# Optimization experiments

Hardware: AMD Instinct MI355X
Metric: run time of the kernel (lower is better)

Reference implementation:

```python
import jax, jax.numpy as jnp
import numpy as np

N, LH, PL = 512, 20, 10          # agents, history len, prediction len
H, E, NH, FF = 128, 64, 10, 2048  # rnn hidden, embedding, heads, ffn dim
D = H + 2                         # transformer d_model = 130
DH = D // NH                      # head dim = 13
DT = 0.1
NLAYERS = 3


def setup_inputs() -> dict:
    key = jax.random.key(0)
    ks = list(jax.random.split(key, 40))
    def rn(shape, s=0.02):
        return jax.random.normal(ks.pop(), shape, jnp.float32) * s
    Tracks = jax.random.normal(ks.pop(), (N, LH, 5), jnp.float32)
    Tracks = Tracks.at[:, :, 0].set(1.0)  # nonzero ids: all agents active every frame
    return dict(
        Tracks=Tracks,
        W_emb=rn((E, 4)), b_emb=jnp.zeros((E,), jnp.float32),
        W_ih=rn((4 * H, E)), W_hh=rn((4 * H, H)),
        b_ih=jnp.zeros((4 * H,), jnp.float32), b_hh=jnp.zeros((4 * H,), jnp.float32),
        enc_qkv_w=rn((NLAYERS, 3 * D, D)), enc_qkv_b=jnp.zeros((NLAYERS, 3 * D), jnp.float32),
        enc_out_w=rn((NLAYERS, D, D)), enc_out_b=jnp.zeros((NLAYERS, D), jnp.float32),
        enc_ff1_w=rn((NLAYERS, FF, D)), enc_ff1_b=jnp.zeros((NLAYERS, FF), jnp.float32),
        enc_ff2_w=rn((NLAYERS, D, FF)), enc_ff2_b=jnp.zeros((NLAYERS, D), jnp.float32),
        enc_ln1_s=jnp.ones((NLAYERS, D), jnp.float32), enc_ln1_b=jnp.zeros((NLAYERS, D), jnp.float32),
        enc_ln2_s=jnp.ones((NLAYERS, D), jnp.float32), enc_ln2_b=jnp.zeros((NLAYERS, D), jnp.float32),
        W_sp=rn((H, D)), b_sp=jnp.zeros((H,), jnp.float32),
        W_p1=rn((H, H)), b_p1=jnp.zeros((H,), jnp.float32),
        W_p2=rn((H, H)), b_p2=jnp.zeros((H,), jnp.float32),
        W_pl=rn((2, H)), b_pl=jnp.zeros((2,), jnp.float32),
    )


def _ln(x, s, b):
    m = jnp.mean(x, -1, keepdims=True)
    v = jnp.mean((x - m) ** 2, -1, keepdims=True)
    return (x - m) / jnp.sqrt(v + 1e-5) * s + b


def _mha(x, qkv_w, qkv_b, ow, ob):
    # x: [N, D] unbatched sequence of N agent tokens (torch unbatched semantics)
    qkv = x @ qkv_w.T + qkv_b
    q, k, v = jnp.split(qkv, 3, -1)
    def heads(t):
        return t.reshape(-1, NH, DH).transpose(1, 0, 2)  # [NH, N, DH]
    q, k, v = heads(q), heads(k), heads(v)
    scores = jnp.einsum('hnd,hmd->hnm', q, k) / jnp.sqrt(jnp.float32(DH))
    att = jax.nn.softmax(scores, -1)
    o = jnp.einsum('hnm,hmd->hnd', att, v).transpose(1, 0, 2).reshape(-1, D)
    return o @ ow.T + ob


def _forward(Tracks, W_emb, b_emb, W_ih, W_hh, b_ih, b_hh,
             enc_qkv_w, enc_qkv_b, enc_out_w, enc_out_b,
             enc_ff1_w, enc_ff1_b, enc_ff2_w, enc_ff2_b,
             enc_ln1_s, enc_ln1_b, enc_ln2_s, enc_ln2_b,
             W_sp, b_sp, W_p1, b_p1, W_p2, b_p2, W_pl, b_pl):
    def emb(x):
        return x @ W_emb.T + b_emb

    def lstm(x, h, c):  # torch LSTMCell, gate order i,f,g,o
        g = x @ W_ih.T + b_ih + h @ W_hh.T + b_hh
        i, f, gg, o = jnp.split(g, 4, -1)
        c2 = jax.nn.sigmoid(f) * c + jax.nn.sigmoid(i) * jnp.tanh(gg)
        return jax.nn.sigmoid(o) * jnp.tanh(c2), c2

    def sp(h, pos):  # sp_model: 3-layer post-norm transformer encoder + linear
        x = jnp.concatenate([h, pos], 1)  # [N, D]
        for j in range(NLAYERS):
            a = _mha(x, enc_qkv_w[j], enc_qkv_b[j], enc_out_w[j], enc_out_b[j])
            x = _ln(x + a, enc_ln1_s[j], enc_ln1_b[j])
            f = jax.nn.relu(x @ enc_ff1_w[j].T + enc_ff1_b[j]) @ enc_ff2_w[j].T + enc_ff2_b[j]
            x = _ln(x + f, enc_ln2_s[j], enc_ln2_b[j])
        return x @ W_sp.T + b_sp

    def rm_sp(inp, Sh, c):
        h2, c2 = lstm(emb(inp), Sh, c)
        return sp(h2, inp[:, :2]), c2

    n = Tracks.shape[0]
    inp0 = Tracks[:, 0, 1:]
    z = jnp.zeros((n, H), Tracks.dtype)
    h, c = lstm(emb(inp0), z, z)  # step-0 init (original processes step 0 twice)
    Sh = sp(h, inp0[:, :2])

    def step(carry, inp):
        Sh, c = carry
        Sh, c = rm_sp(inp, Sh, c)
        return (Sh, c), None

    (Sh, c), _ = jax.lax.scan(step, (Sh, c), jnp.moveaxis(Tracks[:, :, 1:], 1, 0))

    def pstep(carry, _):
        Sh, c, cf = carry
        x = jax.nn.relu(Sh @ W_p1.T + b_p1) + Sh
        x = jax.nn.relu(x @ W_p2.T + b_p2) + x
        a = x @ W_pl.T + b_pl                       # acceleration [N,2]
        v = a * DT + cf[:, 2:]                      # velocity update first (in-place order)
        pnew = a * (DT * DT / 2) + v * DT + cf[:, :2]
        out = jnp.concatenate([pnew, v], 1)
        Sh, c = rm_sp(out, Sh, c)
        return (Sh, c, out), out

    _, pre = jax.lax.scan(pstep, (Sh, c, Tracks[:, -1, 1:]), None, length=PL)
    return jnp.moveaxis(pre, 0, 1)  # [N, pre_len, 4]


def reference(Tracks, W_emb, b_emb, W_ih, W_hh, b_ih, b_hh,
              enc_qkv_w, enc_qkv_b, enc_out_w, enc_out_b,
              enc_ff1_w, enc_ff1_b, enc_ff2_w, enc_ff2_b,
              enc_ln1_s, enc_ln1_b, enc_ln2_s, enc_ln2_b,
              W_sp, b_sp, W_p1, b_p1, W_p2, b_p2, W_pl, b_pl):
    return _forward(Tracks, W_emb, b_emb, W_ih, W_hh, b_ih, b_hh,
                    enc_qkv_w, enc_qkv_b, enc_out_w, enc_out_b,
                    enc_ff1_w, enc_ff1_b, enc_ff2_w, enc_ff2_b,
                    enc_ln1_s, enc_ln1_b, enc_ln2_s, enc_ln2_b,
                    W_sp, b_sp, W_p1, b_p1, W_p2, b_p2, W_pl, b_pl)
```

## Files before the change

kernel.cpp:

```cpp
#include <hip/hip_runtime.h>


#define Nn 512
#define Dd 130
#define DP 132
#define Hh 128
#define Ee 64
#define FFf 2048
#define KG 192
#define TS 68

typedef float v4 __attribute__((ext_vector_type(4)));
typedef float v2 __attribute__((ext_vector_type(2)));

struct Args {
  const float *Tracks, *W_emb, *b_emb, *W_ih, *W_hh, *b_ih, *b_hh;
  const float *qkv_w, *qkv_b, *out_w, *out_b, *ff1_w, *ff1_b, *ff2_w, *ff2_b;
  const float *ln1_s, *ln1_b, *ln2_s, *ln2_b;
  const float *W_sp, *b_sp, *W_p1, *b_p1, *W_p2, *b_p2, *W_pl, *b_pl;
  float *X, *T, *Q, *Kb, *V, *O, *Sh, *C, *X1, *X2, *Y, *PART, *outp;
};

__device__ __forceinline__ float sigm(float x){ return 1.f/(1.f+__expf(-x)); }

__global__ __launch_bounds__(512) void k_proj(Args a){
  int rg = blockIdx.x & 7, cs = blockIdx.x >> 3;
  int r0 = rg*64, c0 = cs*64;
  __shared__ alignas(16) float xs[Dd*TS];
  __shared__ alignas(16) float ws[Dd*TS];
  int tid = threadIdx.x, cg = tid & 15, ig = tid >> 4;
  for (int idx=tid; idx<64*Dd; idx+=512){ int i=idx/Dd, j=idx-i*Dd; xs[j*TS+i] = a.X[(r0+i)*DP+j]; }
  for (int idx=tid; idx<64*Dd; idx+=512){ int c=idx/Dd, j=idx-c*Dd; ws[j*TS+c] = a.W_sp[(c0+c)*Dd+j]; }
  __syncthreads();
  float acc[2][4] = {};
  const float* xp = xs + 2*ig;
  const float* wp = ws + 4*cg;
  #pragma unroll 4
  for (int j=0;j<Dd;j++){
    v2 xv = *(const v2*)(xp + j*TS);
    v4 wv = *(const v4*)(wp + j*TS);
    #pragma unroll
    for (int aa=0;aa<2;aa++)
      #pragma unroll
      for (int bb=0;bb<4;bb++) acc[aa][bb] += xv[aa]*wv[bb];
  }
  #pragma unroll
  for (int aa=0;aa<2;aa++){
    int r = r0 + 2*ig + aa, c = c0 + 4*cg;
    v4 o; 
    #pragma unroll
    for (int bb=0;bb<4;bb++) o[bb] = acc[aa][bb] + a.b_sp[c+bb];
    *(v4*)&a.Sh[r*Hh+c] = o;
  }
}

__global__ __launch_bounds__(512) void k_mlp(Args a, const float* inp, const float* W, const float* b, float* outp){
  int rg = blockIdx.x & 7, cs = blockIdx.x >> 3;
  int r0 = rg*64, c0 = cs*64;
  __shared__ alignas(16) float xs[Hh*TS];
  __shared__ alignas(16) float ws[Hh*TS];
  int tid = threadIdx.x, cg = tid & 15, ig = tid >> 4;
  for (int idx=tid; idx<64*Hh; idx+=512){ int i=idx>>7, j=idx&127; xs[j*TS+i] = inp[(r0+i)*Hh+j]; }
  for (int idx=tid; idx<64*Hh; idx+=512){ int c=idx>>7, j=idx&127; ws[j*TS+c] = W[(c0+c)*Hh+j]; }
  __syncthreads();
  float acc[2][4] = {};
  const float* xp = xs + 2*ig;
  const float* wp = ws + 4*cg;
  #pragma unroll 4
  for (int j=0;j<Hh;j++){
    v2 xv = *(const v2*)(xp + j*TS);
    v4 wv = *(const v4*)(wp + j*TS);
    #pragma unroll
    for (int aa=0;aa<2;aa++)
      #pragma unroll
      for (int bb=0;bb<4;bb++) acc[aa][bb] += xv[aa]*wv[bb];
  }
  #pragma unroll
  for (int aa=0;aa<2;aa++){
    int r = r0 + 2*ig + aa, c = c0 + 4*cg;
    v4 ri = *(const v4*)&inp[r*Hh+c];
    v4 o;
    #pragma unroll
    for (int bb=0;bb<4;bb++) o[bb] = fmaxf(acc[aa][bb]+b[c+bb],0.f) + ri[bb];
    *(v4*)&outp[r*Hh+c] = o;
  }
}

__global__ __launch_bounds__(256) void k_pout(Args a, int p){
  int r0 = blockIdx.x*8;
  __shared__ float red[16*17];
  int tid = threadIdx.x;
  int o = tid & 15, kq = tid >> 4;
  int ii = o>>1, jj = o&1, r = r0+ii;
  float s = 0.f;
  for (int v=kq*8; v<kq*8+8; v++) s += a.X2[r*Hh+v]*a.W_pl[jj*Hh+v];
  red[o*17+kq] = s;
  __syncthreads();
  if (tid < 16){
    int oo=tid, i2=oo>>1, j=oo&1, rr=r0+i2;
    float av = a.b_pl[j];
    for (int k=0;k<16;k++) av += red[oo*17+k];
    float cf0, cf2;
    if (p==0){ cf0 = a.Tracks[(rr*20+19)*5+1+j]; cf2 = a.Tracks[(rr*20+19)*5+3+j]; }
    else     { cf0 = a.outp[rr*40+(p-1)*4+j];    cf2 = a.outp[rr*40+(p-1)*4+2+j]; }
    float vv = av*0.1f + cf2;
    float pn = av*0.005f + vv*0.1f + cf0;
    a.outp[rr*40+p*4+j]   = pn;
    a.outp[rr*40+p*4+2+j] = vv;
  }
}

__global__ __launch_bounds__(512) void k_gates(Args a, int xin_mode, int tstep, int p, int sh_zero){
  int rg = blockIdx.x & 7, us = blockIdx.x >> 3;
  int r0 = rg*64, u0 = us*16;
  __shared__ alignas(16) float xs[KG*TS];
  __shared__ alignas(16) float ws[KG*TS];
  __shared__ float xin[64*4];
  int tid = threadIdx.x, cg = tid & 15, ig = tid >> 4;
  for (int idx=tid; idx<64*4; idx+=512){ int i=idx>>2, j=idx&3; int r=r0+i;
    xin[i*4+j] = (xin_mode==0) ? a.Tracks[(r*20+tstep)*5+1+j] : a.outp[r*40+p*4+j]; }
  for (int idx=tid; idx<64*Hh; idx+=512){ int i=idx>>7, v=idx&127;
    xs[(Ee+v)*TS+i] = sh_zero ? 0.f : a.Sh[(r0+i)*Hh+v]; }
  for (int idx=tid; idx<64*KG; idx+=512){ int row=idx/KG, j=idx-row*KG;
    int u=row>>2, g=row&3; int wrow = g*Hh + u0 + u;
    ws[j*TS+row] = (j<Ee) ? a.W_ih[wrow*Ee+j] : a.W_hh[wrow*Hh+(j-Ee)]; }
  __syncthreads();
  for (int idx=tid; idx<64*Ee; idx+=512){ int e=idx>>6, i=idx&63;
    float s = a.b_emb[e];
    #pragma unroll
    for (int j=0;j<4;j++) s += xin[i*4+j]*a.W_emb[e*4+j];
    xs[e*TS+i] = s; }
  __syncthreads();
  float acc[2][4] = {};
  const float* xp = xs + 2*ig;
  const float* wp = ws + 4*cg;
  #pragma unroll 4
  for (int j=0;j<KG;j++){
    v2 xv = *(const v2*)(xp + j*TS);
    v4 wv = *(const v4*)(wp + j*TS);
    #pragma unroll
    for (int aa=0;aa<2;aa++)
      #pragma unroll
      for (int bb=0;bb<4;bb++) acc[aa][bb] += xv[aa]*wv[bb];
  }
  int u = u0 + cg;
  #pragma unroll
  for (int rr=0;rr<2;rr++){
    int r = r0 + 2*ig + rr;
    float gi = acc[rr][0] + a.b_ih[u]      + a.b_hh[u];
    float gf = acc[rr][1] + a.b_ih[Hh+u]   + a.b_hh[Hh+u];
    float gg = acc[rr][2] + a.b_ih[2*Hh+u] + a.b_hh[2*Hh+u];
    float go = acc[rr][3] + a.b_ih[3*Hh+u] + a.b_hh[3*Hh+u];
    float cp = sh_zero ? 0.f : a.C[r*Hh+u];
    float c2 = sigm(gf)*cp + sigm(gi)*tanhf(gg);
    a.C[r*Hh+u] = c2;
    a.X[r*DP+u] = sigm(go)*tanhf(c2);
  }
  if (us==0 && tid<128){ int i=tid>>1, jj=tid&1;
    a.X[(r0+i)*DP + Hh + jj] = xin[i*4+jj]; }
}

__global__ __launch_bounds__(512) void k_qkv(Args a, int layer){
  int rg = blockIdx.x & 7, cs = blockIdx.x >> 3;
  int r0 = rg*64, c0 = cs*64;
  __shared__ alignas(16) float xs[Dd*TS];
  __shared__ alignas(16) float ws[Dd*TS];
  const float* qw = a.qkv_w + layer*390*Dd;
  const float* qb = a.qkv_b + layer*390;
  int tid = threadIdx.x, cg = tid & 15, ig = tid >> 4;
  for (int idx=tid; idx<64*Dd; idx+=512){ int i=idx/Dd, j=idx-i*Dd; xs[j*TS+i] = a.X[(r0+i)*DP+j]; }
  for (int idx=tid; idx<64*Dd; idx+=512){ int c=idx/Dd, j=idx-c*Dd; int gc=c0+c;
    ws[j*TS+c] = (gc<390) ? qw[gc*Dd+j] : 0.f; }
  __syncthreads();
  float acc[2][4] = {};
  const float* xp = xs + 2*ig;
  const float* wp = ws + 4*cg;
  #pragma unroll 4
  for (int j=0;j<Dd;j++){
    v2 xv = *(const v2*)(xp + j*TS);
    v4 wv = *(const v4*)(wp + j*TS);
    #pragma unroll
    for (int aa=0;aa<2;aa++)
      #pragma unroll
      for (int bb=0;bb<4;bb++) acc[aa][bb] += xv[aa]*wv[bb];
  }
  #pragma unroll
  for (int aa=0;aa<2;aa++){
    int r = r0 + 2*ig + aa;
    #pragma unroll
    for (int bb=0;bb<4;bb++){
      int c = c0 + 4*cg + bb;
      if (c < 390){
        float v = acc[aa][bb] + qb[c];
        if (c < Dd)        a.Q [r*DP + c]        = v;
        else if (c < 2*Dd) a.Kb[r*DP + (c-Dd)]   = v;
        else               a.V [r*DP + (c-2*Dd)] = v;
      }
    }
  }
}

__global__ __launch_bounds__(256) void k_attn(Args a){
  int rg = blockIdx.x & 31, head = blockIdx.x >> 5;
  int r0 = rg*16, hc = head*13;
  __shared__ alignas(16) float kv[512*14];
  __shared__ alignas(16) float sc[16*516];
  __shared__ float red[16*17];
  __shared__ float rowm[16], rowsi[16];
  int tid = threadIdx.x;
  const float scale = rsqrtf(13.f);
  for (int idx=tid; idx<512*13; idx+=256){ int m=idx/13, d=idx-13*m; kv[m*14+d]=a.Kb[m*DP+hc+d]; }
  __syncthreads();
  { int ii=tid>>4, mg=tid&15;
    float q[13];
    #pragma unroll
    for (int d=0;d<13;d++) q[d]=a.Q[(r0+ii)*DP+hc+d]*scale;
    for (int k=0;k<32;k++){ int m=mg+16*k;
      float s=0.f;
      #pragma unroll
      for (int d=0;d<13;d++) s += q[d]*kv[m*14+d];
      sc[ii*516+m]=s; } }
  __syncthreads();
  for (int idx=tid; idx<512*13; idx+=256){ int m=idx/13, d=idx-13*m; kv[d*524+m]=a.V[m*DP+hc+d]; }
  { int row=tid>>4, l=tid&15; float mx=-1e30f;
    for (int k=0;k<32;k++) mx=fmaxf(mx, sc[row*516+l+16*k]);
    red[row*17+l]=mx; }
  __syncthreads();
  if (tid<16){ float mx=-1e30f; for(int k=0;k<16;k++) mx=fmaxf(mx,red[tid*17+k]); rowm[tid]=mx; }
  __syncthreads();
  { int row=tid>>4, l=tid&15; float s=0.f; float mx=rowm[row];
    for (int k=0;k<32;k++){ int m=l+16*k; float e=__expf(sc[row*516+m]-mx); sc[row*516+m]=e; s+=e; }
    red[row*17+l]=s; }
  __syncthreads();
  if (tid<16){ float s=0.f; for(int k=0;k<16;k++) s+=red[tid*17+k]; rowsi[tid]=1.f/s; }
  __syncthreads();
  if (tid<208){ int ii=tid/13, d=tid-13*ii;
    float accv=0.f;
    const float* sp = sc + ii*516;
    const float* vp = kv + d*524;
    #pragma unroll 4
    for (int mb=0;mb<128;mb++){
      v4 sv = *(const v4*)(sp + 4*mb);
      v4 vv = *(const v4*)(vp + 4*mb);
      accv += sv[0]*vv[0]+sv[1]*vv[1]+sv[2]*vv[2]+sv[3]*vv[3];
    }
    a.O[(r0+ii)*DP+hc+d]=accv*rowsi[ii]; }
}

__global__ __launch_bounds__(512) void k_oproj(Args a, int layer){
  int rg = blockIdx.x & 7, cs = blockIdx.x >> 3;
  int r0 = rg*64, c0 = cs*64;
  __shared__ alignas(16) float xs[Dd*TS];
  __shared__ alignas(16) float ws[Dd*TS];
  const float* ow = a.out_w + layer*Dd*Dd;
  const float* ob = a.out_b + layer*Dd;
  int tid = threadIdx.x, cg = tid & 15, ig = tid >> 4;
  for (int idx=tid; idx<64*Dd; idx+=512){ int i=idx/Dd, j=idx-i*Dd; xs[j*TS+i]=a.O[(r0+i)*DP+j]; }
  for (int idx=tid; idx<64*Dd; idx+=512){ int c=idx/Dd, j=idx-c*Dd; int gc=c0+c;
    ws[j*TS+c] = (gc<Dd) ? ow[gc*Dd+j] : 0.f; }
  __syncthreads();
  float acc[2][4] = {};
  const float* xp = xs + 2*ig;
  const float* wp = ws + 4*cg;
  #pragma unroll 4
  for (int j=0;j<Dd;j++){
    v2 xv = *(const v2*)(xp + j*TS);
    v4 wv = *(const v4*)(wp + j*TS);
    #pragma unroll
    for (int aa=0;aa<2;aa++)
      #pragma unroll
      for (int bb=0;bb<4;bb++) acc[aa][bb] += xv[aa]*wv[bb];
  }
  #pragma unroll
  for (int aa=0;aa<2;aa++){
    int r = r0 + 2*ig + aa;
    #pragma unroll
    for (int bb=0;bb<4;bb++){
      int c = c0 + 4*cg + bb;
      if (c < Dd) a.T[r*DP+c] = acc[aa][bb] + ob[c] + a.X[r*DP+c];
    }
  }
}

__global__ __launch_bounds__(256) void k_ln(Args a, const float* s, const float* b, int mode_ff, int layer){
  int r0 = blockIdx.x*8;
  __shared__ float row[8*132];
  __shared__ float red1[8*33], red2[8*33];
  __shared__ float mu[8], inv[8];
  int tid = threadIdx.x, i = tid>>5, l = tid&31;
  if (mode_ff==0){
    for (int idx=tid; idx<8*Dd; idx+=256){ int ii=idx/Dd, c=idx-ii*Dd; row[ii*132+c]=a.T[(r0+ii)*DP+c]; }
  } else {
    const float* f2b = a.ff2_b + layer*Dd;
    for (int idx=tid; idx<8*Dd; idx+=256){ int ii=idx/Dd, c=idx-ii*Dd;
      float sum = a.X[(r0+ii)*DP+c] + f2b[c];
      for (int ksl=0;ksl<16;ksl++) sum += a.PART[(ksl*Nn + r0+ii)*DP + c];
      row[ii*132+c]=sum; }
  }
  __syncthreads();
  { float s1=0.f, s2=0.f;
    for (int k=0;k<5;k++){ int c=l+32*k; if(c<Dd){ float v=row[i*132+c]; s1+=v; s2+=v*v; } }
    red1[i*33+l]=s1; red2[i*33+l]=s2; }
  __syncthreads();
  if (tid<8){ float s1=0.f,s2=0.f; for(int k=0;k<32;k++){ s1+=red1[tid*33+k]; s2+=red2[tid*33+k]; }
    float m=s1/130.f; mu[tid]=m; inv[tid]=rsqrtf(s2/130.f - m*m + 1e-5f); }
  __syncthreads();
  for (int idx=tid; idx<8*Dd; idx+=256){ int ii=idx/Dd, c=idx-ii*Dd;
    a.X[(r0+ii)*DP+c] = (row[ii*132+c]-mu[ii])*inv[ii]*s[c] + b[c]; }
}

__global__ __launch_bounds__(512) void k_ff1(Args a, int layer){
  int rg = blockIdx.x & 7, cs = blockIdx.x >> 3;
  int r0 = rg*64, c0 = cs*64;
  __shared__ alignas(16) float xs[Dd*TS];
  __shared__ alignas(16) float ws[Dd*TS];
  const float* w1 = a.ff1_w + layer*FFf*Dd;
  const float* b1 = a.ff1_b + layer*FFf;
  int tid = threadIdx.x, cg = tid & 15, ig = tid >> 4;
  for (int idx=tid; idx<64*Dd; idx+=512){ int i=idx/Dd, j=idx-i*Dd; xs[j*TS+i]=a.X[(r0+i)*DP+j]; }
  for (int idx=tid; idx<64*Dd; idx+=512){ int c=idx/Dd, j=idx-c*Dd; ws[j*TS+c]=w1[(c0+c)*Dd+j]; }
  __syncthreads();
  float acc[2][4] = {};
  const float* xp = xs + 2*ig;
  const float* wp = ws + 4*cg;
  #pragma unroll 4
  for (int j=0;j<Dd;j++){
    v2 xv = *(const v2*)(xp + j*TS);
    v4 wv = *(const v4*)(wp + j*TS);
    #pragma unroll
    for (int aa=0;aa<2;aa++)
      #pragma unroll
      for (int bb=0;bb<4;bb++) acc[aa][bb] += xv[aa]*wv[bb];
  }
  #pragma unroll
  for (int aa=0;aa<2;aa++){
    int r = r0 + 2*ig + aa, c = c0 + 4*cg;
    v4 o;
    #pragma unroll
    for (int bb=0;bb<4;bb++) o[bb] = fmaxf(acc[aa][bb]+b1[c+bb],0.f);
    *(v4*)&a.Y[r*FFf+c] = o;
  }
}

__global__ __launch_bounds__(512) void k_ff2(Args a, int layer){
  int b = blockIdx.x;
  int rg = b & 7; int t = b >> 3; int ks = t/3; int cs = t - ks*3;
  int r0 = rg*64, c0 = cs*64, k0 = ks*128;
  __shared__ alignas(16) float xs[128*TS];
  __shared__ alignas(16) float ws[128*TS];
  const float* w2 = a.ff2_w + layer*Dd*FFf;
  int tid = threadIdx.x, cg = tid & 15, ig = tid >> 4;
  for (int idx=tid; idx<64*128; idx+=512){ int i=idx>>7, j=idx&127; xs[j*TS+i]=a.Y[(r0+i)*FFf+k0+j]; }
  for (int idx=tid; idx<64*128; idx+=512){ int c=idx>>7, j=idx&127; int gc=c0+c;
    ws[j*TS+c] = (gc<Dd) ? w2[gc*FFf+k0+j] : 0.f; }
  __syncthreads();
  float acc[2][4] = {};
  const float* xp = xs + 2*ig;
  const float* wp = ws + 4*cg;
  #pragma unroll 4
  for (int j=0;j<128;j++){
    v2 xv = *(const v2*)(xp + j*TS);
    v4 wv = *(const v4*)(wp + j*TS);
    #pragma unroll
    for (int aa=0;aa<2;aa++)
      #pragma unroll
      for (int bb=0;bb<4;bb++) acc[aa][bb] += xv[aa]*wv[bb];
  }
  #pragma unroll
  for (int aa=0;aa<2;aa++){
    int r = r0 + 2*ig + aa;
    #pragma unroll
    for (int bb=0;bb<4;bb++){
      int c = c0 + 4*cg + bb;
      if (c < Dd) a.PART[(ks*Nn + r)*DP + c] = acc[aa][bb];
    }
  }
}

extern "C" void kernel_launch(void* const* d_in, const int* in_sizes, int n_in,
                              void* d_out, int out_size, void* d_ws, size_t ws_size,
                              hipStream_t stream) {
  (void)in_sizes; (void)n_in; (void)out_size; (void)ws_size;
  Args A;
  const float* const* in = (const float* const*)d_in;
  A.Tracks=in[0]; A.W_emb=in[1]; A.b_emb=in[2]; A.W_ih=in[3]; A.W_hh=in[4]; A.b_ih=in[5]; A.b_hh=in[6];
  A.qkv_w=in[7]; A.qkv_b=in[8]; A.out_w=in[9]; A.out_b=in[10];
  A.ff1_w=in[11]; A.ff1_b=in[12]; A.ff2_w=in[13]; A.ff2_b=in[14];
  A.ln1_s=in[15]; A.ln1_b=in[16]; A.ln2_s=in[17]; A.ln2_b=in[18];
  A.W_sp=in[19]; A.b_sp=in[20]; A.W_p1=in[21]; A.b_p1=in[22]; A.W_p2=in[23]; A.b_p2=in[24];
  A.W_pl=in[25]; A.b_pl=in[26];
  float* ws = (float*)d_ws;
  A.X   = ws;
  A.T   = ws + 67584;
  A.Q   = ws + 135168;
  A.Kb  = ws + 202752;
  A.V   = ws + 270336;
  A.O   = ws + 337920;
  A.Sh  = ws + 405504;
  A.C   = ws + 471040;
  A.X1  = ws + 536576;
  A.X2  = ws + 602112;
  A.Y   = ws + 667648;
  A.PART= ws + 1716224;
  A.outp = (float*)d_out;

  dim3 B5(512), B2(256);
  auto enc = [&](){
    for (int l=0;l<3;l++){
      k_qkv  <<<dim3(56),  B5, 0, stream>>>(A, l);
      k_attn <<<dim3(320), B2, 0, stream>>>(A);
      k_oproj<<<dim3(24),  B5, 0, stream>>>(A, l);
      k_ln   <<<dim3(64),  B2, 0, stream>>>(A, A.ln1_s+l*Dd, A.ln1_b+l*Dd, 0, l);
      k_ff1  <<<dim3(256), B5, 0, stream>>>(A, l);
      k_ff2  <<<dim3(384), B5, 0, stream>>>(A, l);
      k_ln   <<<dim3(64),  B2, 0, stream>>>(A, A.ln2_s+l*Dd, A.ln2_b+l*Dd, 1, l);
    }
  };

  k_gates<<<dim3(64), B5, 0, stream>>>(A, 0, 0, 0, 1);
  enc();
  for (int t=0;t<20;t++){
    k_proj <<<dim3(16), B5, 0, stream>>>(A);
    k_gates<<<dim3(64), B5, 0, stream>>>(A, 0, t, 0, 0);
    enc();
  }
  for (int p=0;p<10;p++){
    k_proj<<<dim3(16), B5, 0, stream>>>(A);
    k_mlp <<<dim3(16), B5, 0, stream>>>(A, A.Sh, A.W_p1, A.b_p1, A.X1);
    k_mlp <<<dim3(16), B5, 0, stream>>>(A, A.X1, A.W_p2, A.b_p2, A.X2);
    k_pout<<<dim3(64), B2, 0, stream>>>(A, p);
    if (p < 9){
      k_gates<<<dim3(64), B5, 0, stream>>>(A, 1, 0, p, 0);
      enc();
    }
  }
}
```

Measured before the change: 9.059 ms.

## Fuse all stage kernels into one persistent kernel with grid-wide barriers

Replaces the long sequence of small kernel launches (hundreds per forward) with a single persistent 256-block kernel. Each former kernel becomes a device phase that loops over virtual blocks, with an atomic-counter grid barrier between phases. Attention now uses 512 threads with split reductions, and ff2 uses a 2-chunk K split to halve partial sums. This removes launch overhead and inter-kernel gaps. In exchange every phase pays a spin-wait barrier, and small phases leave most blocks idle at lower occupancy (one 512-thread block per CU).

```diff
diff --git a/kernel.cpp b/kernel.cpp
--- a/kernel.cpp
+++ b/kernel.cpp
@@ -7,8 +7,9 @@
 #define Hh 128
 #define Ee 64
 #define FFf 2048
-#define KG 192
 #define TS 68
+#define NB 256
+#define NT 512
 
 typedef float v4 __attribute__((ext_vector_type(4)));
 typedef float v2 __attribute__((ext_vector_type(2)));
@@ -19,18 +20,19 @@
   const float *ln1_s, *ln1_b, *ln2_s, *ln2_b;
   const float *W_sp, *b_sp, *W_p1, *b_p1, *W_p2, *b_p2, *W_pl, *b_pl;
   float *X, *T, *Q, *Kb, *V, *O, *Sh, *C, *X1, *X2, *Y, *PART, *outp;
+  unsigned *bar;
 };
 
 __device__ __forceinline__ float sigm(float x){ return 1.f/(1.f+__expf(-x)); }
 
-__global__ __launch_bounds__(512) void k_proj(Args a){
-  int rg = blockIdx.x & 7, cs = blockIdx.x >> 3;
+__device__ __forceinline__ void ph_proj(const Args& a, float* sm, int vb){
+  int rg = vb & 7, cs = vb >> 3;
   int r0 = rg*64, c0 = cs*64;
-  __shared__ alignas(16) float xs[Dd*TS];
-  __shared__ alignas(16) float ws[Dd*TS];
-  int tid = threadIdx.x, cg = tid & 15, ig = tid >> 4;
-  for (int idx=tid; idx<64*Dd; idx+=512){ int i=idx/Dd, j=idx-i*Dd; xs[j*TS+i] = a.X[(r0+i)*DP+j]; }
-  for (int idx=tid; idx<64*Dd; idx+=512){ int c=idx/Dd, j=idx-c*Dd; ws[j*TS+c] = a.W_sp[(c0+c)*Dd+j]; }
+  float* xs = sm; float* ws = sm + 13056;
+  int tid = threadIdx.x, cg = tid & 15, ig = tid >> 4;
+  __syncthreads();
+  for (int idx=tid; idx<64*Dd; idx+=NT){ int i=idx/Dd, j=idx-i*Dd; xs[j*TS+i] = a.X[(r0+i)*DP+j]; }
+  for (int idx=tid; idx<64*Dd; idx+=NT){ int c=idx/Dd, j=idx-c*Dd; ws[j*TS+c] = a.W_sp[(c0+c)*Dd+j]; }
   __syncthreads();
   float acc[2][4] = {};
   const float* xp = xs + 2*ig;
@@ -47,21 +49,22 @@
   #pragma unroll
   for (int aa=0;aa<2;aa++){
     int r = r0 + 2*ig + aa, c = c0 + 4*cg;
-    v4 o; 
+    v4 o;
     #pragma unroll
     for (int bb=0;bb<4;bb++) o[bb] = acc[aa][bb] + a.b_sp[c+bb];
     *(v4*)&a.Sh[r*Hh+c] = o;
   }
 }
 
-__global__ __launch_bounds__(512) void k_mlp(Args a, const float* inp, const float* W, const float* b, float* outp){
-  int rg = blockIdx.x & 7, cs = blockIdx.x >> 3;
+__device__ __forceinline__ void ph_mlp(const Args& a, float* sm, int vb,
+                                       const float* inp, const float* W, const float* b, float* outp){
+  int rg = vb & 7, cs = vb >> 3;
   int r0 = rg*64, c0 = cs*64;
-  __shared__ alignas(16) float xs[Hh*TS];
-  __shared__ alignas(16) float ws[Hh*TS];
-  int tid = threadIdx.x, cg = tid & 15, ig = tid >> 4;
-  for (int idx=tid; idx<64*Hh; idx+=512){ int i=idx>>7, j=idx&127; xs[j*TS+i] = inp[(r0+i)*Hh+j]; }
-  for (int idx=tid; idx<64*Hh; idx+=512){ int c=idx>>7, j=idx&127; ws[j*TS+c] = W[(c0+c)*Hh+j]; }
+  float* xs = sm; float* ws = sm + 13056;
+  int tid = threadIdx.x, cg = tid & 15, ig = tid >> 4;
+  __syncthreads();
+  for (int idx=tid; idx<64*Hh; idx+=NT){ int i=idx>>7, j=idx&127; xs[j*TS+i] = inp[(r0+i)*Hh+j]; }
+  for (int idx=tid; idx<64*Hh; idx+=NT){ int c=idx>>7, j=idx&127; ws[j*TS+c] = W[(c0+c)*Hh+j]; }
   __syncthreads();
   float acc[2][4] = {};
   const float* xp = xs + 2*ig;
@@ -86,15 +89,18 @@
   }
 }
 
-__global__ __launch_bounds__(256) void k_pout(Args a, int p){
-  int r0 = blockIdx.x*8;
-  __shared__ float red[16*17];
+__device__ __forceinline__ void ph_pout(const Args& a, float* sm, int vb, int p){
+  float* red = sm;
+  int r0 = vb*8;
   int tid = threadIdx.x;
-  int o = tid & 15, kq = tid >> 4;
-  int ii = o>>1, jj = o&1, r = r0+ii;
-  float s = 0.f;
-  for (int v=kq*8; v<kq*8+8; v++) s += a.X2[r*Hh+v]*a.W_pl[jj*Hh+v];
-  red[o*17+kq] = s;
+  __syncthreads();
+  if (tid < 256){
+    int o = tid & 15, kq = tid >> 4;
+    int ii = o>>1, jj = o&1, r = r0+ii;
+    float s = 0.f;
+    for (int v=kq*8; v<kq*8+8; v++) s += a.X2[r*Hh+v]*a.W_pl[jj*Hh+v];
+    red[o*17+kq] = s;
+  }
   __syncthreads();
   if (tid < 16){
     int oo=tid, i2=oo>>1, j=oo&1, rr=r0+i2;
@@ -110,38 +116,47 @@
   }
 }
 
-__global__ __launch_bounds__(512) void k_gates(Args a, int xin_mode, int tstep, int p, int sh_zero){
-  int rg = blockIdx.x & 7, us = blockIdx.x >> 3;
+__device__ __forceinline__ void ph_gates(const Args& a, float* sm, int vb,
+                                         int xin_mode, int tstep, int p, int sh_zero){
+  int rg = vb & 7, us = vb >> 3;
   int r0 = rg*64, u0 = us*16;
-  __shared__ alignas(16) float xs[KG*TS];
-  __shared__ alignas(16) float ws[KG*TS];
-  __shared__ float xin[64*4];
-  int tid = threadIdx.x, cg = tid & 15, ig = tid >> 4;
-  for (int idx=tid; idx<64*4; idx+=512){ int i=idx>>2, j=idx&3; int r=r0+i;
+  float* xs = sm;
+  float* ws = sm + 6528;
+  float* xin = sm + 13056;
+  int tid = threadIdx.x, cg = tid & 15, ig = tid >> 4;
+  __syncthreads();
+  for (int idx=tid; idx<64*4; idx+=NT){ int i=idx>>2, j=idx&3; int r=r0+i;
     xin[i*4+j] = (xin_mode==0) ? a.Tracks[(r*20+tstep)*5+1+j] : a.outp[r*40+p*4+j]; }
-  for (int idx=tid; idx<64*Hh; idx+=512){ int i=idx>>7, v=idx&127;
-    xs[(Ee+v)*TS+i] = sh_zero ? 0.f : a.Sh[(r0+i)*Hh+v]; }
-  for (int idx=tid; idx<64*KG; idx+=512){ int row=idx/KG, j=idx-row*KG;
-    int u=row>>2, g=row&3; int wrow = g*Hh + u0 + u;
-    ws[j*TS+row] = (j<Ee) ? a.W_ih[wrow*Ee+j] : a.W_hh[wrow*Hh+(j-Ee)]; }
-  __syncthreads();
-  for (int idx=tid; idx<64*Ee; idx+=512){ int e=idx>>6, i=idx&63;
-    float s = a.b_emb[e];
-    #pragma unroll
-    for (int j=0;j<4;j++) s += xin[i*4+j]*a.W_emb[e*4+j];
-    xs[e*TS+i] = s; }
-  __syncthreads();
-  float acc[2][4] = {};
-  const float* xp = xs + 2*ig;
-  const float* wp = ws + 4*cg;
-  #pragma unroll 4
-  for (int j=0;j<KG;j++){
-    v2 xv = *(const v2*)(xp + j*TS);
-    v4 wv = *(const v4*)(wp + j*TS);
-    #pragma unroll
-    for (int aa=0;aa<2;aa++)
-      #pragma unroll
-      for (int bb=0;bb<4;bb++) acc[aa][bb] += xv[aa]*wv[bb];
+  float acc[2][4] = {};
+  for (int ch=0; ch<2; ch++){
+    __syncthreads();
+    for (int idx=tid; idx<96*64; idx+=NT){ int kk=idx>>6, i=idx&63; int k=ch*96+kk;
+      float v;
+      if (k < Ee){
+        v = a.b_emb[k];
+        #pragma unroll
+        for (int j=0;j<4;j++) v += xin[i*4+j]*a.W_emb[k*4+j];
+      } else {
+        v = sh_zero ? 0.f : a.Sh[(r0+i)*Hh + (k-Ee)];
+      }
+      xs[kk*TS+i] = v;
+    }
+    for (int idx=tid; idx<96*64; idx+=NT){ int kk=idx>>6, row=idx&63; int k=ch*96+kk;
+      int u=row>>2, g=row&3; int wrow = g*Hh + u0 + u;
+      ws[kk*TS+row] = (k<Ee) ? a.W_ih[wrow*Ee+k] : a.W_hh[wrow*Hh+(k-Ee)];
+    }
+    __syncthreads();
+    const float* xp = xs + 2*ig;
+    const float* wp = ws + 4*cg;
+    #pragma unroll 4
+    for (int jj=0;jj<96;jj++){
+      v2 xv = *(const v2*)(xp + jj*TS);
+      v4 wv = *(const v4*)(wp + jj*TS);
+      #pragma unroll
+      for (int aa=0;aa<2;aa++)
+        #pragma unroll
+        for (int bb=0;bb<4;bb++) acc[aa][bb] += xv[aa]*wv[bb];
+    }
   }
   int u = u0 + cg;
   #pragma unroll
@@ -160,16 +175,16 @@
     a.X[(r0+i)*DP + Hh + jj] = xin[i*4+jj]; }
 }
 
-__global__ __launch_bounds__(512) void k_qkv(Args a, int layer){
-  int rg = blockIdx.x & 7, cs = blockIdx.x >> 3;
+__device__ __forceinline__ void ph_qkv(const Args& a, float* sm, int vb, int layer){
+  int rg = vb & 7, cs = vb >> 3;
   int r0 = rg*64, c0 = cs*64;
-  __shared__ alignas(16) float xs[Dd*TS];
-  __shared__ alignas(16) float ws[Dd*TS];
+  float* xs = sm; float* ws = sm + 13056;
   const float* qw = a.qkv_w + layer*390*Dd;
   const float* qb = a.qkv_b + layer*390;
   int tid = threadIdx.x, cg = tid & 15, ig = tid >> 4;
-  for (int idx=tid; idx<64*Dd; idx+=512){ int i=idx/Dd, j=idx-i*Dd; xs[j*TS+i] = a.X[(r0+i)*DP+j]; }
-  for (int idx=tid; idx<64*Dd; idx+=512){ int c=idx/Dd, j=idx-c*Dd; int gc=c0+c;
+  __syncthreads();
+  for (int idx=tid; idx<64*Dd; idx+=NT){ int i=idx/Dd, j=idx-i*Dd; xs[j*TS+i] = a.X[(r0+i)*DP+j]; }
+  for (int idx=tid; idx<64*Dd; idx+=NT){ int c=idx/Dd, j=idx-c*Dd; int gc=c0+c;
     ws[j*TS+c] = (gc<390) ? qw[gc*Dd+j] : 0.f; }
   __syncthreads();
   float acc[2][4] = {};
@@ -200,63 +215,69 @@
   }
 }
 
-__global__ __launch_bounds__(256) void k_attn(Args a){
-  int rg = blockIdx.x & 31, head = blockIdx.x >> 5;
+__device__ __forceinline__ void ph_attn(const Args& a, float* sm, int vb){
+  float* kv    = sm;
+  float* sc    = sm + 7168;
+  float* red   = sm + 15424;
+  float* rowm  = sm + 15952;
+  float* rowsi = sm + 15968;
+  float* red2  = sm + 15984;
+  int rg = vb & 31, head = vb >> 5;
   int r0 = rg*16, hc = head*13;
-  __shared__ alignas(16) float kv[512*14];
-  __shared__ alignas(16) float sc[16*516];
-  __shared__ float red[16*17];
-  __shared__ float rowm[16], rowsi[16];
   int tid = threadIdx.x;
   const float scale = rsqrtf(13.f);
-  for (int idx=tid; idx<512*13; idx+=256){ int m=idx/13, d=idx-13*m; kv[m*14+d]=a.Kb[m*DP+hc+d]; }
-  __syncthreads();
-  { int ii=tid>>4, mg=tid&15;
+  __syncthreads();
+  for (int idx=tid; idx<512*13; idx+=NT){ int m=idx/13, d=idx-13*m; kv[m*14+d]=a.Kb[m*DP+hc+d]; }
+  __syncthreads();
+  { int ii=tid>>5, mg=tid&31;
     float q[13];
     #pragma unroll
     for (int d=0;d<13;d++) q[d]=a.Q[(r0+ii)*DP+hc+d]*scale;
-    for (int k=0;k<32;k++){ int m=mg+16*k;
+    for (int k=0;k<16;k++){ int m=mg+32*k;
       float s=0.f;
       #pragma unroll
       for (int d=0;d<13;d++) s += q[d]*kv[m*14+d];
       sc[ii*516+m]=s; } }
   __syncthreads();
-  for (int idx=tid; idx<512*13; idx+=256){ int m=idx/13, d=idx-13*m; kv[d*524+m]=a.V[m*DP+hc+d]; }
-  { int row=tid>>4, l=tid&15; float mx=-1e30f;
-    for (int k=0;k<32;k++) mx=fmaxf(mx, sc[row*516+l+16*k]);
-    red[row*17+l]=mx; }
-  __syncthreads();
-  if (tid<16){ float mx=-1e30f; for(int k=0;k<16;k++) mx=fmaxf(mx,red[tid*17+k]); rowm[tid]=mx; }
-  __syncthreads();
-  { int row=tid>>4, l=tid&15; float s=0.f; float mx=rowm[row];
-    for (int k=0;k<32;k++){ int m=l+16*k; float e=__expf(sc[row*516+m]-mx); sc[row*516+m]=e; s+=e; }
-    red[row*17+l]=s; }
-  __syncthreads();
-  if (tid<16){ float s=0.f; for(int k=0;k<16;k++) s+=red[tid*17+k]; rowsi[tid]=1.f/s; }
-  __syncthreads();
-  if (tid<208){ int ii=tid/13, d=tid-13*ii;
+  for (int idx=tid; idx<512*13; idx+=NT){ int m=idx/13, d=idx-13*m; kv[d*524+m]=a.V[m*DP+hc+d]; }
+  { int row=tid>>5, l=tid&31; float mx=-1e30f;
+    for (int k=0;k<16;k++) mx=fmaxf(mx, sc[row*516+l+32*k]);
+    red[row*33+l]=mx; }
+  __syncthreads();
+  if (tid<16){ float mx=-1e30f; for(int k=0;k<32;k++) mx=fmaxf(mx,red[tid*33+k]); rowm[tid]=mx; }
+  __syncthreads();
+  { int row=tid>>5, l=tid&31; float s=0.f; float mx=rowm[row];
+    for (int k=0;k<16;k++){ int m=l+32*k; float e=__expf(sc[row*516+m]-mx); sc[row*516+m]=e; s+=e; }
+    red[row*33+l]=s; }
+  __syncthreads();
+  if (tid<16){ float s=0.f; for(int k=0;k<32;k++) s+=red[tid*33+k]; rowsi[tid]=1.f/s; }
+  __syncthreads();
+  if (tid<416){ int pid=tid>>1, h=tid&1; int ii=pid/13, d=pid-13*ii;
+    const float* sp = sc + ii*516 + h*256;
+    const float* vp = kv + d*524 + h*256;
     float accv=0.f;
-    const float* sp = sc + ii*516;
-    const float* vp = kv + d*524;
     #pragma unroll 4
-    for (int mb=0;mb<128;mb++){
+    for (int mb=0;mb<64;mb++){
       v4 sv = *(const v4*)(sp + 4*mb);
       v4 vv = *(const v4*)(vp + 4*mb);
       accv += sv[0]*vv[0]+sv[1]*vv[1]+sv[2]*vv[2]+sv[3]*vv[3];
     }
-    a.O[(r0+ii)*DP+hc+d]=accv*rowsi[ii]; }
-}
-
-__global__ __launch_bounds__(512) void k_oproj(Args a, int layer){
-  int rg = blockIdx.x & 7, cs = blockIdx.x >> 3;
+    red2[pid*2+h]=accv; }
+  __syncthreads();
+  if (tid<208){ int ii=tid/13, d=tid-13*ii;
+    a.O[(r0+ii)*DP+hc+d]=(red2[tid*2]+red2[tid*2+1])*rowsi[ii]; }
+}
+
+__device__ __forceinline__ void ph_oproj(const Args& a, float* sm, int vb, int layer){
+  int rg = vb & 7, cs = vb >> 3;
   int r0 = rg*64, c0 = cs*64;
-  __shared__ alignas(16) float xs[Dd*TS];
-  __shared__ alignas(16) float ws[Dd*TS];
+  float* xs = sm; float* ws = sm + 13056;
   const float* ow = a.out_w + layer*Dd*Dd;
   const float* ob = a.out_b + layer*Dd;
   int tid = threadIdx.x, cg = tid & 15, ig = tid >> 4;
-  for (int idx=tid; idx<64*Dd; idx+=512){ int i=idx/Dd, j=idx-i*Dd; xs[j*TS+i]=a.O[(r0+i)*DP+j]; }
-  for (int idx=tid; idx<64*Dd; idx+=512){ int c=idx/Dd, j=idx-c*Dd; int gc=c0+c;
+  __syncthreads();
+  for (int idx=tid; idx<64*Dd; idx+=NT){ int i=idx/Dd, j=idx-i*Dd; xs[j*TS+i]=a.O[(r0+i)*DP+j]; }
+  for (int idx=tid; idx<64*Dd; idx+=NT){ int c=idx/Dd, j=idx-c*Dd; int gc=c0+c;
     ws[j*TS+c] = (gc<Dd) ? ow[gc*Dd+j] : 0.f; }
   __syncthreads();
   float acc[2][4] = {};
@@ -282,43 +303,50 @@
   }
 }
 
-__global__ __launch_bounds__(256) void k_ln(Args a, const float* s, const float* b, int mode_ff, int layer){
-  int r0 = blockIdx.x*8;
-  __shared__ float row[8*132];
-  __shared__ float red1[8*33], red2[8*33];
-  __shared__ float mu[8], inv[8];
-  int tid = threadIdx.x, i = tid>>5, l = tid&31;
+__device__ __forceinline__ void ph_ln(const Args& a, float* sm, int vb,
+                                      const float* s, const float* b, int mode_ff, int layer){
+  float* row  = sm;
+  float* red1 = sm + 1056;
+  float* red2 = sm + 1320;
+  float* mu   = sm + 1584;
+  float* inv  = sm + 1592;
+  int r0 = vb*8;
+  int tid = threadIdx.x;
+  __syncthreads();
   if (mode_ff==0){
-    for (int idx=tid; idx<8*Dd; idx+=256){ int ii=idx/Dd, c=idx-ii*Dd; row[ii*132+c]=a.T[(r0+ii)*DP+c]; }
+    for (int idx=tid; idx<8*Dd; idx+=NT){ int ii=idx/Dd, c=idx-ii*Dd; row[ii*132+c]=a.T[(r0+ii)*DP+c]; }
   } else {
     const float* f2b = a.ff2_b + layer*Dd;
-    for (int idx=tid; idx<8*Dd; idx+=256){ int ii=idx/Dd, c=idx-ii*Dd;
+    for (int idx=tid; idx<8*Dd; idx+=NT){ int ii=idx/Dd, c=idx-ii*Dd;
       float sum = a.X[(r0+ii)*DP+c] + f2b[c];
-      for (int ksl=0;ksl<16;ksl++) sum += a.PART[(ksl*Nn + r0+ii)*DP + c];
+      for (int ksl=0;ksl<8;ksl++) sum += a.PART[(ksl*Nn + r0+ii)*DP + c];
       row[ii*132+c]=sum; }
   }
   __syncthreads();
-  { float s1=0.f, s2=0.f;
+  if (tid<256){
+    int i = tid>>5, l = tid&31;
+    float s1=0.f, s2=0.f;
     for (int k=0;k<5;k++){ int c=l+32*k; if(c<Dd){ float v=row[i*132+c]; s1+=v; s2+=v*v; } }
-    red1[i*33+l]=s1; red2[i*33+l]=s2; }
+    red1[i*33+l]=s1; red2[i*33+l]=s2;
+  }
   __syncthreads();
   if (tid<8){ float s1=0.f,s2=0.f; for(int k=0;k<32;k++){ s1+=red1[tid*33+k]; s2+=red2[tid*33+k]; }
     float m=s1/130.f; mu[tid]=m; inv[tid]=rsqrtf(s2/130.f - m*m + 1e-5f); }
   __syncthreads();
-  for (int idx=tid; idx<8*Dd; idx+=256){ int ii=idx/Dd, c=idx-ii*Dd;
+  for (int idx=tid; idx<8*Dd; idx+=NT){ int ii=idx/Dd, c=idx-ii*Dd;
     a.X[(r0+ii)*DP+c] = (row[ii*132+c]-mu[ii])*inv[ii]*s[c] + b[c]; }
 }
 
-__global__ __launch_bounds__(512) void k_ff1(Args a, int layer){
-  int rg = blockIdx.x & 7, cs = blockIdx.x >> 3;
+__device__ __forceinline__ void ph_ff1(const Args& a, float* sm, int vb, int layer){
+  int rg = vb & 7, cs = vb >> 3;
   int r0 = rg*64, c0 = cs*64;
-  __shared__ alignas(16) float xs[Dd*TS];
-  __shared__ alignas(16) float ws[Dd*TS];
+  float* xs = sm; float* ws = sm + 13056;
   const float* w1 = a.ff1_w + layer*FFf*Dd;
   const float* b1 = a.ff1_b + layer*FFf;
   int tid = threadIdx.x, cg = tid & 15, ig = tid >> 4;
-  for (int idx=tid; idx<64*Dd; idx+=512){ int i=idx/Dd, j=idx-i*Dd; xs[j*TS+i]=a.X[(r0+i)*DP+j]; }
-  for (int idx=tid; idx<64*Dd; idx+=512){ int c=idx/Dd, j=idx-c*Dd; ws[j*TS+c]=w1[(c0+c)*Dd+j]; }
+  __syncthreads();
+  for (int idx=tid; idx<64*Dd; idx+=NT){ int i=idx/Dd, j=idx-i*Dd; xs[j*TS+i]=a.X[(r0+i)*DP+j]; }
+  for (int idx=tid; idx<64*Dd; idx+=NT){ int c=idx/Dd, j=idx-c*Dd; ws[j*TS+c]=w1[(c0+c)*Dd+j]; }
   __syncthreads();
   float acc[2][4] = {};
   const float* xp = xs + 2*ig;
@@ -342,29 +370,31 @@
   }
 }
 
-__global__ __launch_bounds__(512) void k_ff2(Args a, int layer){
-  int b = blockIdx.x;
-  int rg = b & 7; int t = b >> 3; int ks = t/3; int cs = t - ks*3;
-  int r0 = rg*64, c0 = cs*64, k0 = ks*128;
-  __shared__ alignas(16) float xs[128*TS];
-  __shared__ alignas(16) float ws[128*TS];
+__device__ __forceinline__ void ph_ff2(const Args& a, float* sm, int vb, int layer){
+  int rg = vb & 7; int t = vb >> 3; int ks = t/3; int cs = t - ks*3;
+  int r0 = rg*64, c0 = cs*64, k0 = ks*256;
+  float* xs = sm; float* ws = sm + 13056;
   const float* w2 = a.ff2_w + layer*Dd*FFf;
   int tid = threadIdx.x, cg = tid & 15, ig = tid >> 4;
-  for (int idx=tid; idx<64*128; idx+=512){ int i=idx>>7, j=idx&127; xs[j*TS+i]=a.Y[(r0+i)*FFf+k0+j]; }
-  for (int idx=tid; idx<64*128; idx+=512){ int c=idx>>7, j=idx&127; int gc=c0+c;
-    ws[j*TS+c] = (gc<Dd) ? w2[gc*FFf+k0+j] : 0.f; }
-  __syncthreads();
-  float acc[2][4] = {};
-  const float* xp = xs + 2*ig;
-  const float* wp = ws + 4*cg;
-  #pragma unroll 4
-  for (int j=0;j<128;j++){
-    v2 xv = *(const v2*)(xp + j*TS);
-    v4 wv = *(const v4*)(wp + j*TS);
-    #pragma unroll
-    for (int aa=0;aa<2;aa++)
-      #pragma unroll
-      for (int bb=0;bb<4;bb++) acc[aa][bb] += xv[aa]*wv[bb];
+  float acc[2][4] = {};
+  for (int ch=0; ch<2; ch++){
+    __syncthreads();
+    int kb = k0 + ch*128;
+    for (int idx=tid; idx<64*128; idx+=NT){ int i=idx>>7, j=idx&127; xs[j*TS+i]=a.Y[(r0+i)*FFf+kb+j]; }
+    for (int idx=tid; idx<64*128; idx+=NT){ int c=idx>>7, j=idx&127; int gc=c0+c;
+      ws[j*TS+c] = (gc<Dd) ? w2[gc*FFf+kb+j] : 0.f; }
+    __syncthreads();
+    const float* xp = xs + 2*ig;
+    const float* wp = ws + 4*cg;
+    #pragma unroll 4
+    for (int j=0;j<128;j++){
+      v2 xv = *(const v2*)(xp + j*TS);
+      v4 wv = *(const v4*)(wp + j*TS);
+      #pragma unroll
+      for (int aa=0;aa<2;aa++)
+        #pragma unroll
+        for (int bb=0;bb<4;bb++) acc[aa][bb] += xv[aa]*wv[bb];
+    }
   }
   #pragma unroll
   for (int aa=0;aa<2;aa++){
@@ -373,6 +403,58 @@
     for (int bb=0;bb<4;bb++){
       int c = c0 + 4*cg + bb;
       if (c < Dd) a.PART[(ks*Nn + r)*DP + c] = acc[aa][bb];
+    }
+  }
+}
+
+#define FORVB(G) for (int vb = (int)blockIdx.x; vb < (G); vb += NB)
+
+__global__ __launch_bounds__(NT, 1) void mega(Args a){
+  __shared__ float sm[21896];
+  unsigned tgt = 0;
+  unsigned* bar = a.bar;
+
+  auto GSYNC = [&](){
+    __syncthreads();
+    if (threadIdx.x == 0){
+      tgt += NB;
+      __threadfence();
+      __hip_atomic_fetch_add(bar, 1u, __ATOMIC_RELAXED, __HIP_MEMORY_SCOPE_AGENT);
+      while (__hip_atomic_load(bar, __ATOMIC_RELAXED, __HIP_MEMORY_SCOPE_AGENT) < tgt){
+        __builtin_amdgcn_s_sleep(1);
+      }
+      __threadfence();
+    }
+    __syncthreads();
+  };
+
+  auto enc = [&](){
+    for (int l=0;l<3;l++){
+      FORVB(56)  ph_qkv  (a, sm, vb, l);                                   GSYNC();
+      FORVB(320) ph_attn (a, sm, vb);                                      GSYNC();
+      FORVB(24)  ph_oproj(a, sm, vb, l);                                   GSYNC();
+      FORVB(64)  ph_ln   (a, sm, vb, a.ln1_s+l*Dd, a.ln1_b+l*Dd, 0, l);    GSYNC();
+      FORVB(256) ph_ff1  (a, sm, vb, l);                                   GSYNC();
+      FORVB(192) ph_ff2  (a, sm, vb, l);                                   GSYNC();
+      FORVB(64)  ph_ln   (a, sm, vb, a.ln2_s+l*Dd, a.ln2_b+l*Dd, 1, l);    GSYNC();
+    }
+  };
+
+  FORVB(64) ph_gates(a, sm, vb, 0, 0, 0, 1);  GSYNC();
+  enc();
+  for (int t=0;t<20;t++){
+    FORVB(16) ph_proj (a, sm, vb);            GSYNC();
+    FORVB(64) ph_gates(a, sm, vb, 0, t, 0, 0); GSYNC();
+    enc();
+  }
+  for (int p=0;p<10;p++){
+    FORVB(16) ph_proj(a, sm, vb);                                  GSYNC();
+    FORVB(16) ph_mlp (a, sm, vb, a.Sh, a.W_p1, a.b_p1, a.X1);      GSYNC();
+    FORVB(16) ph_mlp (a, sm, vb, a.X1, a.W_p2, a.b_p2, a.X2);      GSYNC();
+    FORVB(64) ph_pout(a, sm, vb, p);                               GSYNC();
+    if (p < 9){
+      FORVB(64) ph_gates(a, sm, vb, 1, 0, p, 0);                   GSYNC();
+      enc();
     }
   }
 }
@@ -402,36 +484,9 @@
   A.X2  = ws + 602112;
   A.Y   = ws + 667648;
   A.PART= ws + 1716224;
+  A.bar = (unsigned*)(ws + 2256896);
   A.outp = (float*)d_out;
 
-  dim3 B5(512), B2(256);
-  auto enc = [&](){
-    for (int l=0;l<3;l++){
-      k_qkv  <<<dim3(56),  B5, 0, stream>>>(A, l);
-      k_attn <<<dim3(320), B2, 0, stream>>>(A);
-      k_oproj<<<dim3(24),  B5, 0, stream>>>(A, l);
-      k_ln   <<<dim3(64),  B2, 0, stream>>>(A, A.ln1_s+l*Dd, A.ln1_b+l*Dd, 0, l);
-      k_ff1  <<<dim3(256), B5, 0, stream>>>(A, l);
-      k_ff2  <<<dim3(384), B5, 0, stream>>>(A, l);
-      k_ln   <<<dim3(64),  B2, 0, stream>>>(A, A.ln2_s+l*Dd, A.ln2_b+l*Dd, 1, l);
-    }
-  };
-
-  k_gates<<<dim3(64), B5, 0, stream>>>(A, 0, 0, 0, 1);
-  enc();
-  for (int t=0;t<20;t++){
-    k_proj <<<dim3(16), B5, 0, stream>>>(A);
-    k_gates<<<dim3(64), B5, 0, stream>>>(A, 0, t, 0, 0);
-    enc();
-  }
-  for (int p=0;p<10;p++){
-    k_proj<<<dim3(16), B5, 0, stream>>>(A);
-    k_mlp <<<dim3(16), B5, 0, stream>>>(A, A.Sh, A.W_p1, A.b_p1, A.X1);
-    k_mlp <<<dim3(16), B5, 0, stream>>>(A, A.X1, A.W_p2, A.b_p2, A.X2);
-    k_pout<<<dim3(64), B2, 0, stream>>>(A, p);
-    if (p < 9){
-      k_gates<<<dim3(64), B5, 0, stream>>>(A, 1, 0, p, 0);
-      enc();
-    }
-  }
-}
+  hipMemsetAsync((void*)A.bar, 0, 64, stream);
+  mega<<<dim3(NB), dim3(NT), 0, stream>>>(A);
+}
```

After: 21.54 ms. 2.38x slower.

## Fuse layernorms into FF1 and projection kernels, halve FF2 split-K

Applied to the files above, without the earlier changes.

The post-attention layernorm is folded into the FF1 kernel. Each block recomputes the norm for its 64 rows, and the first column slice writes the normalized X back. The last encoder layer's FF2-reduction layernorm moves into the spatial projection kernel, so two launches per encoder pass are removed. FF2 now covers 256 K-columns per block in two chunks, which halves the split-K partial count and the partial sums reduced afterward. The cost is redundant LN work across column blocks, extra shared memory that may lower occupancy, and fewer FF2 blocks.

```diff
diff --git a/kernel.cpp b/kernel.cpp
--- a/kernel.cpp
+++ b/kernel.cpp
@@ -23,14 +23,36 @@
 
 __device__ __forceinline__ float sigm(float x){ return 1.f/(1.f+__expf(-x)); }
 
+#define LN_REDUCE(SCR) \
+  { int row_=tid>>3, l8=tid&7; float s1=0.f, s2=0.f; \
+    for (int k=0;k<17;k++){ int c=l8+8*k; if(c<Dd){ float v=(SCR)[row_*132+c]; s1+=v; s2+=v*v; } } \
+    red1[row_*9+l8]=s1; red2_[row_*9+l8]=s2; } \
+  __syncthreads(); \
+  if (tid<64){ float s1=0.f,s2=0.f; \
+    for (int k=0;k<8;k++){ s1+=red1[tid*9+k]; s2+=red2_[tid*9+k]; } \
+    float m=s1/130.f; mu[tid]=m; inv[tid]=rsqrtf(s2/130.f-m*m+1e-5f); } \
+  __syncthreads();
+
 __global__ __launch_bounds__(512) void k_proj(Args a){
   int rg = blockIdx.x & 7, cs = blockIdx.x >> 3;
   int r0 = rg*64, c0 = cs*64;
   __shared__ alignas(16) float xs[Dd*TS];
   __shared__ alignas(16) float ws[Dd*TS];
-  int tid = threadIdx.x, cg = tid & 15, ig = tid >> 4;
-  for (int idx=tid; idx<64*Dd; idx+=512){ int i=idx/Dd, j=idx-i*Dd; xs[j*TS+i] = a.X[(r0+i)*DP+j]; }
+  __shared__ float row[64*132];
+  __shared__ float red1[64*9], red2_[64*9], mu[64], inv[64];
+  int tid = threadIdx.x, cg = tid & 15, ig = tid >> 4;
+  const float* f2b = a.ff2_b + 2*Dd;
+  const float* lns = a.ln2_s + 2*Dd;
+  const float* lnb = a.ln2_b + 2*Dd;
   for (int idx=tid; idx<64*Dd; idx+=512){ int c=idx/Dd, j=idx-c*Dd; ws[j*TS+c] = a.W_sp[(c0+c)*Dd+j]; }
+  for (int idx=tid; idx<64*Dd; idx+=512){ int i=idx/Dd, j=idx-i*Dd;
+    float sum = a.X[(r0+i)*DP+j] + f2b[j];
+    for (int ksl=0;ksl<8;ksl++) sum += a.PART[(ksl*Nn + r0+i)*DP + j];
+    row[i*132+j] = sum; }
+  __syncthreads();
+  LN_REDUCE(row)
+  for (int idx=tid; idx<64*Dd; idx+=512){ int i=idx/Dd, j=idx-i*Dd;
+    xs[j*TS+i] = (row[i*132+j]-mu[i])*inv[i]*lns[j] + lnb[j]; }
   __syncthreads();
   float acc[2][4] = {};
   const float* xp = xs + 2*ig;
@@ -47,7 +69,7 @@
   #pragma unroll
   for (int aa=0;aa<2;aa++){
     int r = r0 + 2*ig + aa, c = c0 + 4*cg;
-    v4 o; 
+    v4 o;
     #pragma unroll
     for (int bb=0;bb<4;bb++) o[bb] = acc[aa][bb] + a.b_sp[c+bb];
     *(v4*)&a.Sh[r*Hh+c] = o;
@@ -282,21 +304,17 @@
   }
 }
 
-__global__ __launch_bounds__(256) void k_ln(Args a, const float* s, const float* b, int mode_ff, int layer){
+__global__ __launch_bounds__(256) void k_ln(Args a, const float* s, const float* b, int layer){
   int r0 = blockIdx.x*8;
   __shared__ float row[8*132];
   __shared__ float red1[8*33], red2[8*33];
   __shared__ float mu[8], inv[8];
   int tid = threadIdx.x, i = tid>>5, l = tid&31;
-  if (mode_ff==0){
-    for (int idx=tid; idx<8*Dd; idx+=256){ int ii=idx/Dd, c=idx-ii*Dd; row[ii*132+c]=a.T[(r0+ii)*DP+c]; }
-  } else {
-    const float* f2b = a.ff2_b + layer*Dd;
-    for (int idx=tid; idx<8*Dd; idx+=256){ int ii=idx/Dd, c=idx-ii*Dd;
-      float sum = a.X[(r0+ii)*DP+c] + f2b[c];
-      for (int ksl=0;ksl<16;ksl++) sum += a.PART[(ksl*Nn + r0+ii)*DP + c];
-      row[ii*132+c]=sum; }
-  }
+  const float* f2b = a.ff2_b + layer*Dd;
+  for (int idx=tid; idx<8*Dd; idx+=256){ int ii=idx/Dd, c=idx-ii*Dd;
+    float sum = a.X[(r0+ii)*DP+c] + f2b[c];
+    for (int ksl=0;ksl<8;ksl++) sum += a.PART[(ksl*Nn + r0+ii)*DP + c];
+    row[ii*132+c]=sum; }
   __syncthreads();
   { float s1=0.f, s2=0.f;
     for (int k=0;k<5;k++){ int c=l+32*k; if(c<Dd){ float v=row[i*132+c]; s1+=v; s2+=v*v; } }
@@ -314,11 +332,21 @@
   int r0 = rg*64, c0 = cs*64;
   __shared__ alignas(16) float xs[Dd*TS];
   __shared__ alignas(16) float ws[Dd*TS];
+  __shared__ float row[64*132];
+  __shared__ float red1[64*9], red2_[64*9], mu[64], inv[64];
   const float* w1 = a.ff1_w + layer*FFf*Dd;
   const float* b1 = a.ff1_b + layer*FFf;
-  int tid = threadIdx.x, cg = tid & 15, ig = tid >> 4;
-  for (int idx=tid; idx<64*Dd; idx+=512){ int i=idx/Dd, j=idx-i*Dd; xs[j*TS+i]=a.X[(r0+i)*DP+j]; }
+  const float* lns = a.ln1_s + layer*Dd;
+  const float* lnb = a.ln1_b + layer*Dd;
+  int tid = threadIdx.x, cg = tid & 15, ig = tid >> 4;
   for (int idx=tid; idx<64*Dd; idx+=512){ int c=idx/Dd, j=idx-c*Dd; ws[j*TS+c]=w1[(c0+c)*Dd+j]; }
+  for (int idx=tid; idx<64*Dd; idx+=512){ int i=idx/Dd, j=idx-i*Dd; row[i*132+j]=a.T[(r0+i)*DP+j]; }
+  __syncthreads();
+  LN_REDUCE(row)
+  for (int idx=tid; idx<64*Dd; idx+=512){ int i=idx/Dd, j=idx-i*Dd;
+    float v = (row[i*132+j]-mu[i])*inv[i]*lns[j] + lnb[j];
+    xs[j*TS+i] = v;
+    if (cs==0) a.X[(r0+i)*DP+j] = v; }
   __syncthreads();
   float acc[2][4] = {};
   const float* xp = xs + 2*ig;
@@ -345,26 +373,30 @@
 __global__ __launch_bounds__(512) void k_ff2(Args a, int layer){
   int b = blockIdx.x;
   int rg = b & 7; int t = b >> 3; int ks = t/3; int cs = t - ks*3;
-  int r0 = rg*64, c0 = cs*64, k0 = ks*128;
+  int r0 = rg*64, c0 = cs*64, k0 = ks*256;
   __shared__ alignas(16) float xs[128*TS];
   __shared__ alignas(16) float ws[128*TS];
   const float* w2 = a.ff2_w + layer*Dd*FFf;
   int tid = threadIdx.x, cg = tid & 15, ig = tid >> 4;
-  for (int idx=tid; idx<64*128; idx+=512){ int i=idx>>7, j=idx&127; xs[j*TS+i]=a.Y[(r0+i)*FFf+k0+j]; }
-  for (int idx=tid; idx<64*128; idx+=512){ int c=idx>>7, j=idx&127; int gc=c0+c;
-    ws[j*TS+c] = (gc<Dd) ? w2[gc*FFf+k0+j] : 0.f; }
-  __syncthreads();
-  float acc[2][4] = {};
-  const float* xp = xs + 2*ig;
-  const float* wp = ws + 4*cg;
-  #pragma unroll 4
-  for (int j=0;j<128;j++){
-    v2 xv = *(const v2*)(xp + j*TS);
-    v4 wv = *(const v4*)(wp + j*TS);
-    #pragma unroll
-    for (int aa=0;aa<2;aa++)
-      #pragma unroll
-      for (int bb=0;bb<4;bb++) acc[aa][bb] += xv[aa]*wv[bb];
+  float acc[2][4] = {};
+  for (int ch=0; ch<2; ch++){
+    __syncthreads();
+    int kb = k0 + ch*128;
+    for (int idx=tid; idx<64*128; idx+=512){ int i=idx>>7, j=idx&127; xs[j*TS+i]=a.Y[(r0+i)*FFf+kb+j]; }
+    for (int idx=tid; idx<64*128; idx+=512){ int c=idx>>7, j=idx&127; int gc=c0+c;
+      ws[j*TS+c] = (gc<Dd) ? w2[gc*FFf+kb+j] : 0.f; }
+    __syncthreads();
+    const float* xp = xs + 2*ig;
+    const float* wp = ws + 4*cg;
+    #pragma unroll 4
+    for (int j=0;j<128;j++){
+      v2 xv = *(const v2*)(xp + j*TS);
+      v4 wv = *(const v4*)(wp + j*TS);
+      #pragma unroll
+      for (int aa=0;aa<2;aa++)
+        #pragma unroll
+        for (int bb=0;bb<4;bb++) acc[aa][bb] += xv[aa]*wv[bb];
+    }
   }
   #pragma unroll
   for (int aa=0;aa<2;aa++){
@@ -410,10 +442,10 @@
       k_qkv  <<<dim3(56),  B5, 0, stream>>>(A, l);
       k_attn <<<dim3(320), B2, 0, stream>>>(A);
       k_oproj<<<dim3(24),  B5, 0, stream>>>(A, l);
-      k_ln   <<<dim3(64),  B2, 0, stream>>>(A, A.ln1_s+l*Dd, A.ln1_b+l*Dd, 0, l);
       k_ff1  <<<dim3(256), B5, 0, stream>>>(A, l);
-      k_ff2  <<<dim3(384), B5, 0, stream>>>(A, l);
-      k_ln   <<<dim3(64),  B2, 0, stream>>>(A, A.ln2_s+l*Dd, A.ln2_b+l*Dd, 1, l);
+      k_ff2  <<<dim3(192), B5, 0, stream>>>(A, l);
+      if (l < 2)
+        k_ln <<<dim3(64),  B2, 0, stream>>>(A, A.ln2_s+l*Dd, A.ln2_b+l*Dd, l);
     }
   };
 
```

New measurement: 9.365 ms. +3.4%, slower.
